# Optimization experiments

Measured on AMD Instinct MI355X. Metric: run time of the kernel, lower is better.

Reference implementation:

```python
import jax, jax.numpy as jnp
import numpy as np

NORM_CLAMP = 1e-4  # matches torch .clamp(min=0.0001) on the pairwise norm


def _kernel_rbf(x, y, w):
    # x: [B, N, D], y: [B, M, D], w: [B, 1, 1]
    x2 = jnp.sum(x * x, axis=-1)                      # [B, N]
    y2 = jnp.sum(y * y, axis=-1)                      # [B, M]
    xy = jnp.einsum('bnd,bmd->bnm', x, y)             # [B, N, M]
    sq = x2[:, :, None] + y2[:, None, :] - 2.0 * xy
    norm = jnp.sqrt(jnp.maximum(sq, 0.0))
    norm = jnp.maximum(norm, NORM_CLAMP)              # [B, N, M]
    d = x.shape[-1]
    return jnp.exp(-w * norm / d)                     # w broadcasts [B,1,1]


def setup_inputs() -> dict:
    key = jax.random.key(0)
    k1, k2, k3 = jax.random.split(key, 3)
    B, N, D = 32, 256, 32
    x = jax.random.normal(k1, (B, N, D), dtype=jnp.float32)
    y = jax.random.normal(k2, (B, N, D), dtype=jnp.float32)
    w = jax.random.uniform(k3, (B, 1, 1), dtype=jnp.float32)  # per-batch RBF bandwidth (= 1/delta_st)
    return {"x": x, "y": y, "w": w}


def reference(x, y, w):
    # _loss_mmd: mean over batch of per-batch MMD^2 estimates
    k_xx = _kernel_rbf(x, x, w)
    k_yy = _kernel_rbf(y, y, w)
    k_xy = _kernel_rbf(x, y, w)
    per_batch = (k_xx.mean(axis=(1, 2)) + k_yy.mean(axis=(1, 2))
                 - 2.0 * k_xy.mean(axis=(1, 2)))
    return per_batch.mean()
```

## Files before the change

### kernel.cpp

```cpp
#include <hip/hip_runtime.h>
#include <math.h>

#define BB 32
#define NN 256
#define DD 32
#define TPB 256
#define NBLK (BB * 3 * 4 * 4)
#define NPART NBLK

typedef short  bf16x8 __attribute__((ext_vector_type(8)));
typedef short  s16x4  __attribute__((ext_vector_type(4)));
typedef float  f32x4  __attribute__((ext_vector_type(4)));

__device__ __forceinline__ short bf16hi(float x, float& hf) {
    unsigned u = __float_as_uint(x);
    unsigned r = (u + 0x7fffu + ((u >> 16) & 1u)) >> 16;
    hf = __uint_as_float(r << 16);
    return (short)r;
}

__global__ __launch_bounds__(TPB) void mmd_mfma(
    const float* __restrict__ x, const float* __restrict__ y,
    const float* __restrict__ w, float* __restrict__ partials) {
    const int blk = blockIdx.x;
    const int b   = blk / 48;
    int rem = blk - b * 48;
    const int type = rem >> 4;
    rem &= 15;
    const int iq = rem >> 2;
    const int jq = rem & 3;
    const int tid  = threadIdx.x;
    const int wv   = tid >> 6;
    const int lane = tid & 63;

    const float* Abase = (type == 1) ? y : x;
    const float* Bbase = (type == 0) ? x : y;
    const float* Aq = Abase + ((size_t)b * NN + iq * 64) * DD;
    const float* Bq = Bbase + ((size_t)b * NN + jq * 64) * DD;

    __shared__ bf16x8 Ah[4 * 64], Al[4 * 64], Bh[4 * 64], Bl[4 * 64];
    __shared__ float a2s[64], b2s[64];

    #pragma unroll
    for (int u = 0; u < 2; ++u) {
        const int e   = tid + u * 256;
        const int row = e >> 3;
        const int kq  = e & 7;
        const int g   = kq >> 1;
        const int kk  = (kq & 1) * 4;
        const int l   = g * 16 + (row & 15);
        const int it  = row >> 4;
        {
            float4 v = ((const float4*)Aq)[e];
            float h0, h1, h2, h3, d;
            s16x4 hi, lo;
            hi[0] = bf16hi(v.x, h0); lo[0] = bf16hi(v.x - h0, d);
            hi[1] = bf16hi(v.y, h1); lo[1] = bf16hi(v.y - h1, d);
            hi[2] = bf16hi(v.z, h2); lo[2] = bf16hi(v.z - h2, d);
            hi[3] = bf16hi(v.w, h3); lo[3] = bf16hi(v.w - h3, d);
            *(s16x4*)((short*)&Ah[it * 64 + l] + kk) = hi;
            *(s16x4*)((short*)&Al[it * 64 + l] + kk) = lo;
        }
        {
            float4 v = ((const float4*)Bq)[e];
            float h0, h1, h2, h3, d;
            s16x4 hi, lo;
            hi[0] = bf16hi(v.x, h0); lo[0] = bf16hi(v.x - h0, d);
            hi[1] = bf16hi(v.y, h1); lo[1] = bf16hi(v.y - h1, d);
            hi[2] = bf16hi(v.z, h2); lo[2] = bf16hi(v.z - h2, d);
            hi[3] = bf16hi(v.w, h3); lo[3] = bf16hi(v.w - h3, d);
            *(s16x4*)((short*)&Bh[it * 64 + l] + kk) = hi;
            *(s16x4*)((short*)&Bl[it * 64 + l] + kk) = lo;
        }
    }
    if (tid < 128) {
        const int r = tid & 63;
        const float4* rp = (const float4*)((tid < 64 ? Aq : Bq) + (size_t)r * DD);
        float c0 = 0.f, c1 = 0.f, c2 = 0.f, c3 = 0.f;
        #pragma unroll
        for (int k = 0; k < DD / 4; ++k) {
            float4 v = rp[k];
            c0 = fmaf(v.x, v.x, c0);
            c1 = fmaf(v.y, v.y, c1);
            c2 = fmaf(v.z, v.z, c2);
            c3 = fmaf(v.w, v.w, c3);
        }
        (tid < 64 ? a2s : b2s)[r] = (c0 + c1) + (c2 + c3);
    }
    __syncthreads();

    const bf16x8 bh = Bh[wv * 64 + lane];
    const bf16x8 bl = Bl[wv * 64 + lane];
    const float  b2 = b2s[wv * 16 + (lane & 15)];
    const float  negw = -w[b] * (1.0f / (float)DD);
    const bool   sym = (type < 2) && (iq == jq);
    const int    rowbase = (lane >> 4) * 4;
    const int    colr = lane & 15;

    float acc = 0.f;
    #pragma unroll
    for (int it = 0; it < 4; ++it) {
        const bf16x8 ah = Ah[it * 64 + lane];
        const bf16x8 al = Al[it * 64 + lane];
        f32x4 c = {0.f, 0.f, 0.f, 0.f};
        c = __builtin_amdgcn_mfma_f32_16x16x32_bf16(al, bh, c, 0, 0, 0);
        c = __builtin_amdgcn_mfma_f32_16x16x32_bf16(ah, bl, c, 0, 0, 0);
        c = __builtin_amdgcn_mfma_f32_16x16x32_bf16(ah, bh, c, 0, 0, 0);
        const f32x4 a2q = *(const f32x4*)&a2s[it * 16 + rowbase];
        const bool diagt = sym && (it == wv);
        #pragma unroll
        for (int r = 0; r < 4; ++r) {
            float sq = fmaf(-2.0f, c[r], a2q[r] + b2);
            if (diagt && (rowbase + r == colr)) sq = 0.f;
            sq = fmaxf(sq, 1e-8f);
            acc += __expf(negw * __builtin_amdgcn_sqrtf(sq));
        }
    }

    #pragma unroll
    for (int off = 32; off > 0; off >>= 1) acc += __shfl_down(acc, off, 64);
    __shared__ float red[4];
    if (lane == 0) red[wv] = acc;
    __syncthreads();
    if (tid == 0) {
        const float bsum = (red[0] + red[1]) + (red[2] + red[3]);
        const float weight = (type == 2) ? -2.0f : 1.0f;
        const float scale  = weight / ((float)NN * (float)NN * (float)BB);
        partials[blk] = bsum * scale;
    }
}

__global__ __launch_bounds__(256) void mmd_reduce(
    const float* __restrict__ partials, float* __restrict__ out) {
    double acc = 0.0;
    #pragma unroll
    for (int t = 0; t < NPART / 256; ++t)
        acc += (double)partials[threadIdx.x + t * 256];
    #pragma unroll
    for (int off = 32; off > 0; off >>= 1) acc += __shfl_down(acc, off, 64);
    __shared__ double red[4];
    if ((threadIdx.x & 63) == 0) red[threadIdx.x >> 6] = acc;
    __syncthreads();
    if (threadIdx.x == 0)
        out[0] = (float)((red[0] + red[1]) + (red[2] + red[3]));
}

extern "C" void kernel_launch(void* const* d_in, const int* in_sizes, int n_in,
                              void* d_out, int out_size, void* d_ws, size_t ws_size,
                              hipStream_t stream) {
    const float* x = (const float*)d_in[0];
    const float* y = (const float*)d_in[1];
    const float* w = (const float*)d_in[2];
    float* out = (float*)d_out;
    float* partials = (float*)d_ws;

    mmd_mfma<<<NBLK, TPB, 0, stream>>>(x, y, w, partials);
    mmd_reduce<<<1, 256, 0, stream>>>(partials, out);
}
```

Before: 13.12 us.

## Precompute bf16 hi/lo MFMA fragments and norms in a separate prep kernel

Adds a prep kernel that converts x and y once into bf16 hi/lo split fragments, laid out in MFMA operand order, and computes row norms into workspace. The main kernel then loads its fragments directly from global memory with no LDS staging or __syncthreads. This removes the repeated per-tile conversion, which previously ran 3 to 12 times per input tile across blocks. The conversion also uses the hardware v_cvt_pk_bf16_f32 instruction. In exchange it adds a third kernel launch and a workspace round trip of the fragments.

```diff
diff --git a/kernel.cpp b/kernel.cpp
--- a/kernel.cpp
+++ b/kernel.cpp
@@ -4,24 +4,76 @@
 #define BB 32
 #define NN 256
 #define DD 32
-#define TPB 256
 #define NBLK (BB * 3 * 4 * 4)
 #define NPART NBLK
+#define NORM_OFF  4096
+#define FRAG_HI_OFF 32768
+#define FRAG_LO_OFF (32768 + 262144)
 
 typedef short  bf16x8 __attribute__((ext_vector_type(8)));
-typedef short  s16x4  __attribute__((ext_vector_type(4)));
 typedef float  f32x4  __attribute__((ext_vector_type(4)));
 
-__device__ __forceinline__ short bf16hi(float x, float& hf) {
-    unsigned u = __float_as_uint(x);
-    unsigned r = (u + 0x7fffu + ((u >> 16) & 1u)) >> 16;
-    hf = __uint_as_float(r << 16);
-    return (short)r;
+__device__ __forceinline__ unsigned cvt_pk_bf16(float a, float b) {
+    unsigned r;
+    asm("v_cvt_pk_bf16_f32 %0, %1, %2" : "=v"(r) : "v"(a), "v"(b));
+    return r;
 }
 
-__global__ __launch_bounds__(TPB) void mmd_mfma(
+__global__ __launch_bounds__(64) void mmd_prep(
     const float* __restrict__ x, const float* __restrict__ y,
-    const float* __restrict__ w, float* __restrict__ partials) {
+    float* __restrict__ ws) {
+    const int blk  = blockIdx.x;
+    const int b    = blk >> 3;
+    const int side = (blk >> 2) & 1;
+    const int q    = blk & 3;
+    const int r    = q * 64 + threadIdx.x;
+    const float* src = side ? y : x;
+    const float4* rp = (const float4*)(src + ((size_t)b * NN + r) * DD);
+
+    const int p = side * 32 + b;
+    uint4* fh = (uint4*)(ws + FRAG_HI_OFF);
+    uint4* fl = (uint4*)(ws + FRAG_LO_OFF);
+
+    float c0 = 0.f, c1 = 0.f, c2 = 0.f, c3 = 0.f;
+    #pragma unroll
+    for (int g = 0; g < 4; ++g) {
+        const float4 v0 = rp[2 * g], v1 = rp[2 * g + 1];
+        c0 = fmaf(v0.x, v0.x, c0); c1 = fmaf(v0.y, v0.y, c1);
+        c2 = fmaf(v0.z, v0.z, c2); c3 = fmaf(v0.w, v0.w, c3);
+        c0 = fmaf(v1.x, v1.x, c0); c1 = fmaf(v1.y, v1.y, c1);
+        c2 = fmaf(v1.z, v1.z, c2); c3 = fmaf(v1.w, v1.w, c3);
+
+        const unsigned h01 = cvt_pk_bf16(v0.x, v0.y);
+        const unsigned h23 = cvt_pk_bf16(v0.z, v0.w);
+        const unsigned h45 = cvt_pk_bf16(v1.x, v1.y);
+        const unsigned h67 = cvt_pk_bf16(v1.z, v1.w);
+        const float r0 = v0.x - __uint_as_float(h01 << 16);
+        const float r1 = v0.y - __uint_as_float(h01 & 0xffff0000u);
+        const float r2 = v0.z - __uint_as_float(h23 << 16);
+        const float r3 = v0.w - __uint_as_float(h23 & 0xffff0000u);
+        const float r4 = v1.x - __uint_as_float(h45 << 16);
+        const float r5 = v1.y - __uint_as_float(h45 & 0xffff0000u);
+        const float r6 = v1.z - __uint_as_float(h67 << 16);
+        const float r7 = v1.w - __uint_as_float(h67 & 0xffff0000u);
+        const unsigned l01 = cvt_pk_bf16(r0, r1);
+        const unsigned l23 = cvt_pk_bf16(r2, r3);
+        const unsigned l45 = cvt_pk_bf16(r4, r5);
+        const unsigned l67 = cvt_pk_bf16(r6, r7);
+
+        const int slot = (p * 16 + (r >> 4)) * 64 + g * 16 + (r & 15);
+        fh[slot] = make_uint4(h01, h23, h45, h67);
+        fl[slot] = make_uint4(l01, l23, l45, l67);
+    }
+    ws[NORM_OFF + p * NN + r] = (c0 + c1) + (c2 + c3);
+}
+
+__global__ __launch_bounds__(256) void mmd_main(
+    const float* __restrict__ w, float* ws) {
+    const float*  norms = ws + NORM_OFF;
+    const bf16x8* fh = (const bf16x8*)(ws + FRAG_HI_OFF);
+    const bf16x8* fl = (const bf16x8*)(ws + FRAG_LO_OFF);
+    float* partials = ws;
+
     const int blk = blockIdx.x;
     const int b   = blk / 48;
     int rem = blk - b * 48;
@@ -33,65 +85,13 @@
     const int wv   = tid >> 6;
     const int lane = tid & 63;
 
-    const float* Abase = (type == 1) ? y : x;
-    const float* Bbase = (type == 0) ? x : y;
-    const float* Aq = Abase + ((size_t)b * NN + iq * 64) * DD;
-    const float* Bq = Bbase + ((size_t)b * NN + jq * 64) * DD;
+    const int pA = (type == 1 ? 32 : 0) + b;
+    const int pB = (type == 0 ? 0 : 32) + b;
 
-    __shared__ bf16x8 Ah[4 * 64], Al[4 * 64], Bh[4 * 64], Bl[4 * 64];
-    __shared__ float a2s[64], b2s[64];
-
-    #pragma unroll
-    for (int u = 0; u < 2; ++u) {
-        const int e   = tid + u * 256;
-        const int row = e >> 3;
-        const int kq  = e & 7;
-        const int g   = kq >> 1;
-        const int kk  = (kq & 1) * 4;
-        const int l   = g * 16 + (row & 15);
-        const int it  = row >> 4;
-        {
-            float4 v = ((const float4*)Aq)[e];
-            float h0, h1, h2, h3, d;
-            s16x4 hi, lo;
-            hi[0] = bf16hi(v.x, h0); lo[0] = bf16hi(v.x - h0, d);
-            hi[1] = bf16hi(v.y, h1); lo[1] = bf16hi(v.y - h1, d);
-            hi[2] = bf16hi(v.z, h2); lo[2] = bf16hi(v.z - h2, d);
-            hi[3] = bf16hi(v.w, h3); lo[3] = bf16hi(v.w - h3, d);
-            *(s16x4*)((short*)&Ah[it * 64 + l] + kk) = hi;
-            *(s16x4*)((short*)&Al[it * 64 + l] + kk) = lo;
-        }
-        {
-            float4 v = ((const float4*)Bq)[e];
-            float h0, h1, h2, h3, d;
-            s16x4 hi, lo;
-            hi[0] = bf16hi(v.x, h0); lo[0] = bf16hi(v.x - h0, d);
-            hi[1] = bf16hi(v.y, h1); lo[1] = bf16hi(v.y - h1, d);
-            hi[2] = bf16hi(v.z, h2); lo[2] = bf16hi(v.z - h2, d);
-            hi[3] = bf16hi(v.w, h3); lo[3] = bf16hi(v.w - h3, d);
-            *(s16x4*)((short*)&Bh[it * 64 + l] + kk) = hi;
-            *(s16x4*)((short*)&Bl[it * 64 + l] + kk) = lo;
-        }
-    }
-    if (tid < 128) {
-        const int r = tid & 63;
-        const float4* rp = (const float4*)((tid < 64 ? Aq : Bq) + (size_t)r * DD);
-        float c0 = 0.f, c1 = 0.f, c2 = 0.f, c3 = 0.f;
-        #pragma unroll
-        for (int k = 0; k < DD / 4; ++k) {
-            float4 v = rp[k];
-            c0 = fmaf(v.x, v.x, c0);
-            c1 = fmaf(v.y, v.y, c1);
-            c2 = fmaf(v.z, v.z, c2);
-            c3 = fmaf(v.w, v.w, c3);
-        }
-        (tid < 64 ? a2s : b2s)[r] = (c0 + c1) + (c2 + c3);
-    }
-    __syncthreads();
-
-    const bf16x8 bh = Bh[wv * 64 + lane];
-    const bf16x8 bl = Bl[wv * 64 + lane];
-    const float  b2 = b2s[wv * 16 + (lane & 15)];
+    const int bslot = (pB * 16 + jq * 4 + wv) * 64 + lane;
+    const bf16x8 bh = fh[bslot];
+    const bf16x8 bl = fl[bslot];
+    const float  b2 = norms[pB * NN + jq * 64 + wv * 16 + (lane & 15)];
     const float  negw = -w[b] * (1.0f / (float)DD);
     const bool   sym = (type < 2) && (iq == jq);
     const int    rowbase = (lane >> 4) * 4;
@@ -100,13 +100,15 @@
     float acc = 0.f;
     #pragma unroll
     for (int it = 0; it < 4; ++it) {
-        const bf16x8 ah = Ah[it * 64 + lane];
-        const bf16x8 al = Al[it * 64 + lane];
+        const int aslot = (pA * 16 + iq * 4 + it) * 64 + lane;
+        const bf16x8 ah = fh[aslot];
+        const bf16x8 al = fl[aslot];
         f32x4 c = {0.f, 0.f, 0.f, 0.f};
         c = __builtin_amdgcn_mfma_f32_16x16x32_bf16(al, bh, c, 0, 0, 0);
         c = __builtin_amdgcn_mfma_f32_16x16x32_bf16(ah, bl, c, 0, 0, 0);
         c = __builtin_amdgcn_mfma_f32_16x16x32_bf16(ah, bh, c, 0, 0, 0);
-        const f32x4 a2q = *(const f32x4*)&a2s[it * 16 + rowbase];
+        const f32x4 a2q =
+            *(const f32x4*)&norms[pA * NN + iq * 64 + it * 16 + rowbase];
         const bool diagt = sym && (it == wv);
         #pragma unroll
         for (int r = 0; r < 4; ++r) {
@@ -152,8 +154,9 @@
     const float* y = (const float*)d_in[1];
     const float* w = (const float*)d_in[2];
     float* out = (float*)d_out;
-    float* partials = (float*)d_ws;
+    float* ws  = (float*)d_ws;
 
-    mmd_mfma<<<NBLK, TPB, 0, stream>>>(x, y, w, partials);
-    mmd_reduce<<<1, 256, 0, stream>>>(partials, out);
+    mmd_prep<<<BB * 2 * 4, 64, 0, stream>>>(x, y, ws);
+    mmd_main<<<NBLK, 256, 0, stream>>>(w, ws);
+    mmd_reduce<<<1, 256, 0, stream>>>(ws, out);
 }
```

After: 16.56 us. 26.2% more time.

## Exploit kernel-matrix symmetry and use hardware bf16 convert and exp2

Applied to the files above, without the earlier changes.

The self-kernel terms (x-x and y-y) now compute only upper-triangular 64x64 tiles and weight off-diagonal tiles by 2. This cuts blocks per batch from 48 to 36. The manual bf16 rounding is replaced with the packed v_cvt_pk_bf16_f32 instruction, and __expf with a raw v_exp_f32 on a pre-scaled log2e argument. The reduce kernel gains a bounds-checked loop for the new partial count. Symmetric tiles rely on the diagonal zeroing staying correct; the hi/lo split order could change rounding slightly.

```diff
diff --git a/kernel.cpp b/kernel.cpp
--- a/kernel.cpp
+++ b/kernel.cpp
@@ -5,30 +5,48 @@
 #define NN 256
 #define DD 32
 #define TPB 256
-#define NBLK (BB * 3 * 4 * 4)
+#define BPB 36
+#define NBLK (BB * BPB)
 #define NPART NBLK
 
 typedef short  bf16x8 __attribute__((ext_vector_type(8)));
-typedef short  s16x4  __attribute__((ext_vector_type(4)));
 typedef float  f32x4  __attribute__((ext_vector_type(4)));
 
-__device__ __forceinline__ short bf16hi(float x, float& hf) {
-    unsigned u = __float_as_uint(x);
-    unsigned r = (u + 0x7fffu + ((u >> 16) & 1u)) >> 16;
-    hf = __uint_as_float(r << 16);
-    return (short)r;
+__device__ __forceinline__ unsigned cvt_pk_bf16(float a, float b) {
+    unsigned r;
+    asm("v_cvt_pk_bf16_f32 %0, %1, %2" : "=v"(r) : "v"(a), "v"(b));
+    return r;
+}
+__device__ __forceinline__ float fast_sqrt(float x) {
+    float r;
+    asm("v_sqrt_f32 %0, %1" : "=v"(r) : "v"(x));
+    return r;
+}
+__device__ __forceinline__ float fast_exp2(float x) {
+    float r;
+    asm("v_exp_f32 %0, %1" : "=v"(r) : "v"(x));
+    return r;
 }
 
-__global__ __launch_bounds__(TPB) void mmd_mfma(
+__global__ __launch_bounds__(TPB) void mmd_main(
     const float* __restrict__ x, const float* __restrict__ y,
     const float* __restrict__ w, float* __restrict__ partials) {
     const int blk = blockIdx.x;
-    const int b   = blk / 48;
-    int rem = blk - b * 48;
-    const int type = rem >> 4;
-    rem &= 15;
-    const int iq = rem >> 2;
-    const int jq = rem & 3;
+    const int b   = blk / BPB;
+    const int rem = blk - b * BPB;
+    const int type = (rem >= 10) + (rem >= 20);
+    int iq, jq;
+    float weight;
+    if (type == 2) {
+        const int k = rem - 20;
+        iq = k >> 2; jq = k & 3;
+        weight = -2.0f;
+    } else {
+        const int k = rem - type * 10;
+        iq = (k >= 4) + (k >= 7) + (k >= 9);
+        jq = iq + k - ((9 * iq - iq * iq) >> 1);
+        weight = (iq == jq) ? 1.0f : 2.0f;
+    }
     const int tid  = threadIdx.x;
     const int wv   = tid >> 6;
     const int lane = tid & 63;
@@ -47,30 +65,31 @@
         const int row = e >> 3;
         const int kq  = e & 7;
         const int g   = kq >> 1;
-        const int kk  = (kq & 1) * 4;
-        const int l   = g * 16 + (row & 15);
-        const int it  = row >> 4;
+        const int hw  = kq & 1;
+        const int slot = (row >> 4) * 64 + g * 16 + (row & 15);
         {
-            float4 v = ((const float4*)Aq)[e];
-            float h0, h1, h2, h3, d;
-            s16x4 hi, lo;
-            hi[0] = bf16hi(v.x, h0); lo[0] = bf16hi(v.x - h0, d);
-            hi[1] = bf16hi(v.y, h1); lo[1] = bf16hi(v.y - h1, d);
-            hi[2] = bf16hi(v.z, h2); lo[2] = bf16hi(v.z - h2, d);
-            hi[3] = bf16hi(v.w, h3); lo[3] = bf16hi(v.w - h3, d);
-            *(s16x4*)((short*)&Ah[it * 64 + l] + kk) = hi;
-            *(s16x4*)((short*)&Al[it * 64 + l] + kk) = lo;
+            const float4 v = ((const float4*)Aq)[e];
+            const unsigned h01 = cvt_pk_bf16(v.x, v.y);
+            const unsigned h23 = cvt_pk_bf16(v.z, v.w);
+            const float r0 = v.x - __uint_as_float(h01 << 16);
+            const float r1 = v.y - __uint_as_float(h01 & 0xffff0000u);
+            const float r2 = v.z - __uint_as_float(h23 << 16);
+            const float r3 = v.w - __uint_as_float(h23 & 0xffff0000u);
+            ((uint2*)&Ah[slot])[hw] = make_uint2(h01, h23);
+            ((uint2*)&Al[slot])[hw] =
+                make_uint2(cvt_pk_bf16(r0, r1), cvt_pk_bf16(r2, r3));
         }
         {
-            float4 v = ((const float4*)Bq)[e];
-            float h0, h1, h2, h3, d;
-            s16x4 hi, lo;
-            hi[0] = bf16hi(v.x, h0); lo[0] = bf16hi(v.x - h0, d);
-            hi[1] = bf16hi(v.y, h1); lo[1] = bf16hi(v.y - h1, d);
-            hi[2] = bf16hi(v.z, h2); lo[2] = bf16hi(v.z - h2, d);
-            hi[3] = bf16hi(v.w, h3); lo[3] = bf16hi(v.w - h3, d);
-            *(s16x4*)((short*)&Bh[it * 64 + l] + kk) = hi;
-            *(s16x4*)((short*)&Bl[it * 64 + l] + kk) = lo;
+            const float4 v = ((const float4*)Bq)[e];
+            const unsigned h01 = cvt_pk_bf16(v.x, v.y);
+            const unsigned h23 = cvt_pk_bf16(v.z, v.w);
+            const float r0 = v.x - __uint_as_float(h01 << 16);
+            const float r1 = v.y - __uint_as_float(h01 & 0xffff0000u);
+            const float r2 = v.z - __uint_as_float(h23 << 16);
+            const float r3 = v.w - __uint_as_float(h23 & 0xffff0000u);
+            ((uint2*)&Bh[slot])[hw] = make_uint2(h01, h23);
+            ((uint2*)&Bl[slot])[hw] =
+                make_uint2(cvt_pk_bf16(r0, r1), cvt_pk_bf16(r2, r3));
         }
     }
     if (tid < 128) {
@@ -92,7 +111,7 @@
     const bf16x8 bh = Bh[wv * 64 + lane];
     const bf16x8 bl = Bl[wv * 64 + lane];
     const float  b2 = b2s[wv * 16 + (lane & 15)];
-    const float  negw = -w[b] * (1.0f / (float)DD);
+    const float  negw2 = -w[b] * (1.0f / (float)DD) * 1.44269504088896f;
     const bool   sym = (type < 2) && (iq == jq);
     const int    rowbase = (lane >> 4) * 4;
     const int    colr = lane & 15;
@@ -113,7 +132,7 @@
             float sq = fmaf(-2.0f, c[r], a2q[r] + b2);
             if (diagt && (rowbase + r == colr)) sq = 0.f;
             sq = fmaxf(sq, 1e-8f);
-            acc += __expf(negw * __builtin_amdgcn_sqrtf(sq));
+            acc += fast_exp2(negw2 * fast_sqrt(sq));
         }
     }
 
@@ -124,8 +143,7 @@
     __syncthreads();
     if (tid == 0) {
         const float bsum = (red[0] + red[1]) + (red[2] + red[3]);
-        const float weight = (type == 2) ? -2.0f : 1.0f;
-        const float scale  = weight / ((float)NN * (float)NN * (float)BB);
+        const float scale = weight / ((float)NN * (float)NN * (float)BB);
         partials[blk] = bsum * scale;
     }
 }
@@ -134,8 +152,10 @@
     const float* __restrict__ partials, float* __restrict__ out) {
     double acc = 0.0;
     #pragma unroll
-    for (int t = 0; t < NPART / 256; ++t)
-        acc += (double)partials[threadIdx.x + t * 256];
+    for (int t = 0; t < 5; ++t) {
+        const int idx = threadIdx.x + t * 256;
+        if (idx < NPART) acc += (double)partials[idx];
+    }
     #pragma unroll
     for (int off = 32; off > 0; off >>= 1) acc += __shfl_down(acc, off, 64);
     __shared__ double red[4];
@@ -154,6 +174,6 @@
     float* out = (float*)d_out;
     float* partials = (float*)d_ws;
 
-    mmd_mfma<<<NBLK, TPB, 0, stream>>>(x, y, w, partials);
+    mmd_main<<<NBLK, TPB, 0, stream>>>(x, y, w, partials);
     mmd_reduce<<<1, 256, 0, stream>>>(partials, out);
 }
```

Measured after the change: 12.46 us, median of 2. -5.1%, faster.
